# Optimization experiments

Hardware: AMD Instinct MI355X
Metric: run time of the kernel (lower is better)

Reference implementation:

```python
import jax, jax.numpy as jnp
import numpy as np
import math

D_MODEL = 768
NUM_HEADS = 12
HEAD_DIM = D_MODEL // NUM_HEADS
HIDDEN = 3072
EPS = 1e-05
CLAMP = 1e9


def setup_inputs() -> dict:
    key = jax.random.key(0)
    ks = jax.random.split(key, 8)
    s = 0.02
    return {
        "x": jax.random.normal(ks[0], (1, 4096, D_MODEL), dtype=jnp.float32),
        "gamma1": jnp.ones((D_MODEL,), jnp.float32),
        "beta1": jnp.zeros((D_MODEL,), jnp.float32),
        "Wqkv": jax.random.normal(ks[1], (D_MODEL, 3 * D_MODEL), jnp.float32) * s,
        "bqkv": jnp.zeros((3 * D_MODEL,), jnp.float32),
        "Wo": jax.random.normal(ks[2], (D_MODEL, D_MODEL), jnp.float32) * s,
        "bo": jnp.zeros((D_MODEL,), jnp.float32),
        "gamma2": jnp.ones((D_MODEL,), jnp.float32),
        "beta2": jnp.zeros((D_MODEL,), jnp.float32),
        "W1": jax.random.normal(ks[3], (D_MODEL, HIDDEN), jnp.float32) * s,
        "b1": jnp.zeros((HIDDEN,), jnp.float32),
        "W2": jax.random.normal(ks[4], (HIDDEN, D_MODEL), jnp.float32) * s,
        "b2": jnp.zeros((D_MODEL,), jnp.float32),
    }


def layer_norm(x, gamma, beta):
    mean = jnp.mean(x, axis=-1, keepdims=True)
    var = jnp.mean((x - mean) ** 2, axis=-1, keepdims=True)
    y = (x - mean) / jnp.sqrt(var + EPS)
    return gamma * y + beta


def attention_block(x, Wqkv, bqkv, Wo, bo):
    B, S, D = x.shape
    qkv = x @ Wqkv + bqkv                             # [B,S,3D]
    qkv = qkv.reshape(B, S, NUM_HEADS, 3 * HEAD_DIM).transpose(0, 2, 1, 3)  # [B,H,S,3hd]
    q, k, v = jnp.split(qkv, 3, axis=-1)              # each [B,H,S,hd]
    scaled = jnp.einsum("bhqd,bhkd->bhqk", q, k) / math.sqrt(HEAD_DIM)
    causal = jnp.tril(jnp.ones((S, S), dtype=bool))
    scaled = jnp.where(causal, scaled, -jnp.inf)
    scaled = jnp.clip(scaled, -CLAMP, CLAMP)          # torch clamp turns -inf into -1e9
    attn = jax.nn.softmax(scaled, axis=-1)
    vals = jnp.einsum("bhqk,bhkd->bhqd", attn, v)     # [B,H,S,hd]
    vals = vals.transpose(0, 2, 1, 3).reshape(B, S, D)
    return vals @ Wo + bo


def ffn_block(x, W1, b1, W2, b2):
    h = jax.nn.gelu(x @ W1 + b1, approximate=False)
    return h @ W2 + b2


def reference(x, gamma1, beta1, Wqkv, bqkv, Wo, bo, gamma2, beta2, W1, b1, W2, b2):
    x = x + attention_block(layer_norm(x, gamma1, beta1), Wqkv, bqkv, Wo, bo)
    x = x + ffn_block(layer_norm(x, gamma2, beta2), W1, b1, W2, b2)
    return x
```

## Files before the change

kernel.cpp:

```cpp
#include <hip/hip_runtime.h>
#include <hip/hip_bf16.h>
#include <cmath>

using u16 = unsigned short;
typedef __bf16 bf16x8 __attribute__((ext_vector_type(8)));
typedef __bf16 bf16x2 __attribute__((ext_vector_type(2)));
typedef unsigned short u16x8 __attribute__((ext_vector_type(8)));
typedef float f32x4 __attribute__((ext_vector_type(4)));

#define SEQ 4096
#define DM 768
#define NH 12
#define HD 64
#define HID 3072

__device__ __forceinline__ u16 f2bf(float f) {
    union { float f; unsigned u; } v; v.f = f;
    unsigned r = v.u + 0x7fffu + ((v.u >> 16) & 1u);
    return (u16)(r >> 16);
}

__device__ __forceinline__ unsigned pack_bf16(float a, float b) {
    union { bf16x2 v; unsigned u; } c;
    c.v[0] = (__bf16)a; c.v[1] = (__bf16)b;
    return c.u;
}

__device__ __forceinline__ float gelu_exact(float v) {
    float z = fabsf(v) * 0.70710678118654752f;
    float t = __builtin_amdgcn_rcpf(__builtin_fmaf(0.3275911f, z, 1.0f));
    float p = t * __builtin_fmaf(t, __builtin_fmaf(t, __builtin_fmaf(t,
                __builtin_fmaf(t, 1.061405429f, -1.453152027f),
                1.421413741f), -0.284496736f), 0.254829592f);
    float e = __builtin_amdgcn_exp2f(-z * z * 1.44269504088896341f);
    float erfv = __builtin_fmaf(-p, e, 1.0f);
    erfv = (v < 0.0f) ? -erfv : erfv;
    return 0.5f * v * (1.0f + erfv);
}

__device__ __forceinline__ int swz64(int row, int k) {
    return (row << 6) | ((((k >> 3) ^ row) & 7) << 3) | (k & 7);
}
__device__ __forceinline__ int swz128(int row, int k) {
    return (row << 7) | ((((k >> 3) ^ row) & 15) << 3) | (k & 7);
}

__device__ __forceinline__ void ln_row(const float* __restrict__ xr,
                                       const float* __restrict__ g,
                                       const float* __restrict__ b,
                                       u16* __restrict__ yr, int t) {
    float v0 = xr[t], v1 = xr[t + 256], v2 = xr[t + 512];
    float s = v0 + v1 + v2;
#pragma unroll
    for (int m = 32; m; m >>= 1) s += __shfl_xor(s, m);
    __shared__ float red[4], red2[4];
    int wid = t >> 6, lane = t & 63;
    if (lane == 0) red[wid] = s;
    __syncthreads();
    float mean = (red[0] + red[1] + red[2] + red[3]) * (1.0f / DM);
    float d0 = v0 - mean, d1 = v1 - mean, d2 = v2 - mean;
    float q = d0 * d0 + d1 * d1 + d2 * d2;
#pragma unroll
    for (int m = 32; m; m >>= 1) q += __shfl_xor(q, m);
    if (lane == 0) red2[wid] = q;
    __syncthreads();
    float var = (red2[0] + red2[1] + red2[2] + red2[3]) * (1.0f / DM);
    float rstd = rsqrtf(var + 1e-5f);
    yr[t]       = f2bf(d0 * rstd * g[t]       + b[t]);
    yr[t + 256] = f2bf(d1 * rstd * g[t + 256] + b[t + 256]);
    yr[t + 512] = f2bf(d2 * rstd * g[t + 512] + b[t + 512]);
}

__global__ __launch_bounds__(256) void prep_kernel(
    const float* __restrict__ x, const float* __restrict__ g1, const float* __restrict__ b1,
    const float* __restrict__ Wqkv, const float* __restrict__ Wo,
    const float* __restrict__ W1, const float* __restrict__ W2,
    u16* __restrict__ WqkvT, u16* __restrict__ WoT,
    u16* __restrict__ W1T, u16* __restrict__ W2T, u16* __restrict__ y) {
    int bid = blockIdx.x;
    if (bid < 6912) {
        const float* W; u16* Wt; int K, N, ntx, b;
        if (bid < 1728)      { W = Wqkv; Wt = WqkvT; K = 768;  N = 2304; ntx = 72; b = bid; }
        else if (bid < 2304) { W = Wo;   Wt = WoT;   K = 768;  N = 768;  ntx = 24; b = bid - 1728; }
        else if (bid < 4608) { W = W1;   Wt = W1T;   K = 768;  N = 3072; ntx = 96; b = bid - 2304; }
        else                 { W = W2;   Wt = W2T;   K = 3072; N = 768;  ntx = 24; b = bid - 4608; }
        int nb = (b % ntx) * 32, kb = (b / ntx) * 32;
        __shared__ float tile[32][33];
        int tx = threadIdx.x & 31, ty = threadIdx.x >> 5;
#pragma unroll
        for (int i = 0; i < 32; i += 8)
            tile[ty + i][tx] = W[(size_t)(kb + ty + i) * N + nb + tx];
        __syncthreads();
#pragma unroll
        for (int i = 0; i < 32; i += 8)
            Wt[(size_t)(nb + ty + i) * K + kb + tx] = f2bf(tile[tx][ty + i]);
    } else {
        int row = bid - 6912;
        ln_row(x + (size_t)row * DM, g1, b1, y + (size_t)row * DM, threadIdx.x);
    }
}

__global__ __launch_bounds__(256) void vtrans_kernel(const u16* __restrict__ qkv,
                                                     u16* __restrict__ VtG) {
    __shared__ u16 tile[64][68];
    int kvb = blockIdx.x;
    int h = blockIdx.y;
    int t = threadIdx.x;
    int r0 = t >> 3, c0 = (t & 7) << 3;
#pragma unroll
    for (int p = 0; p < 2; ++p) {
        u16x8 v = *reinterpret_cast<const u16x8*>(
            &qkv[(size_t)(kvb * 64 + r0 + p * 32) * 2304 + h * 192 + 128 + c0]);
#pragma unroll
        for (int j = 0; j < 8; ++j)
            tile[r0 + p * 32][c0 + j] = v[j];
    }
    __syncthreads();
    int kv = t & 63, db = (t >> 6) << 4;
#pragma unroll
    for (int i = 0; i < 16; ++i) {
        int d = db + i;
        VtG[(size_t)(h * 64 + d) * SEQ + kvb * 64 + kv] = tile[kv][d];
    }
}

__global__ __launch_bounds__(256) void ln_kernel(const float* __restrict__ x,
                                                 const float* __restrict__ g,
                                                 const float* __restrict__ b,
                                                 u16* __restrict__ y) {
    int row = blockIdx.x;
    ln_row(x + (size_t)row * DM, g, b, y + (size_t)row * DM, threadIdx.x);
}

template<int TM, int TN>
__global__ __launch_bounds__(256) void gemm_bf16(
    const u16* __restrict__ A, const u16* __restrict__ Bt,
    const float* __restrict__ bias, const float* __restrict__ resid,
    float* __restrict__ outF, u16* __restrict__ outB,
    int M, int N, int K, int gelu) {
    constexpr int AP = TM / 32;
    constexpr int BP = TN / 32;
    constexpr int MF = (TN == 128) ? 4 : 2;
    constexpr int NF = 2;
    __shared__ __align__(16) u16 As[2][TM * 64];
    __shared__ __align__(16) u16 Bs[2][TN * 64];
    int tid = threadIdx.x;
    int lane = tid & 63, wid = tid >> 6;
    int lr = lane & 15, hi = lane >> 4;
    int wrow = (TN == 128) ? 0 : (wid >> 1) * 32;
    int wcol = (TN == 128) ? wid * 32 : (wid & 1) * 32;
    int m0 = blockIdx.y * TM, n0 = blockIdx.x * TN;

    f32x4 acc[MF][NF] = {};
    int srow = tid >> 3;
    int sk = (tid & 7) << 3;
    const u16* Ag = A + (size_t)(m0 + srow) * K + sk;
    const u16* Bg = Bt + (size_t)(n0 + srow) * K + sk;

    u16x8 ar[AP], br[BP];
    auto LOAD = [&](int kt) {
#pragma unroll
        for (int p = 0; p < AP; ++p)
            ar[p] = *reinterpret_cast<const u16x8*>(Ag + (size_t)p * 32 * K + kt);
#pragma unroll
        for (int p = 0; p < BP; ++p)
            br[p] = *reinterpret_cast<const u16x8*>(Bg + (size_t)p * 32 * K + kt);
    };
    auto WRITE = [&](int buf) {
#pragma unroll
        for (int p = 0; p < AP; ++p)
            *reinterpret_cast<u16x8*>(&As[buf][swz64(srow + p * 32, sk)]) = ar[p];
#pragma unroll
        for (int p = 0; p < BP; ++p)
            *reinterpret_cast<u16x8*>(&Bs[buf][swz64(srow + p * 32, sk)]) = br[p];
    };

    int NT = K >> 6;
    LOAD(0);
    WRITE(0);
#pragma unroll 2
    for (int t = 0; t < NT; ++t) {
        if (t + 1 < NT) LOAD((t + 1) << 6);
        __syncthreads();
        const u16* as = &As[t & 1][0];
        const u16* bs = &Bs[t & 1][0];
#pragma unroll
        for (int ks = 0; ks < 2; ++ks) {
            bf16x8 af[MF], bfr[NF];
#pragma unroll
            for (int m = 0; m < MF; ++m)
                af[m] = *reinterpret_cast<const bf16x8*>(&as[swz64(wrow + m * 16 + lr, ks * 32 + hi * 8)]);
#pragma unroll
            for (int n = 0; n < NF; ++n)
                bfr[n] = *reinterpret_cast<const bf16x8*>(&bs[swz64(wcol + n * 16 + lr, ks * 32 + hi * 8)]);
            __builtin_amdgcn_s_setprio(1);
#pragma unroll
            for (int m = 0; m < MF; ++m)
#pragma unroll
                for (int n = 0; n < NF; ++n)
                    acc[m][n] = __builtin_amdgcn_mfma_f32_16x16x32_bf16(af[m], bfr[n], acc[m][n], 0, 0, 0);
            __builtin_amdgcn_s_setprio(0);
        }
        if (t + 1 < NT) WRITE((t + 1) & 1);
    }
#pragma unroll
    for (int m = 0; m < MF; ++m) {
#pragma unroll
        for (int n = 0; n < NF; ++n) {
            int col = n0 + wcol + n * 16 + lr;
            float bv = bias[col];
#pragma unroll
            for (int r = 0; r < 4; ++r) {
                int row = m0 + wrow + m * 16 + hi * 4 + r;
                float v = acc[m][n][r] + bv;
                if (gelu) v = gelu_exact(v);
                if (resid) v += resid[(size_t)row * N + col];
                if (outF) outF[(size_t)row * N + col] = v;
                if (outB) outB[(size_t)row * N + col] = f2bf(v);
            }
        }
    }
}

__global__ __launch_bounds__(256, 2) void attn_kernel(const u16* __restrict__ qkv,
                                                      const u16* __restrict__ VtG,
                                                      u16* __restrict__ attn) {
    __shared__ __align__(16) u16 Ks[2][128 * 64];
    __shared__ __align__(16) u16 Vt[2][64 * 128];
    int tid = threadIdx.x;
    int lane = tid & 63, w = tid >> 6;
    int lr = lane & 15, hi = lane >> 4;
    int upper = hi >> 1;
    const float SCL = 0.125f * 1.44269504088896340736f;

    int bid = blockIdx.x;
    int h = bid % NH;
    int qb = (SEQ / 64 - 1) - bid / NH;

    int qrow = qb * 64 + w * 16 + lr;
    bf16x8 qf[2];
#pragma unroll
    for (int ks = 0; ks < 2; ++ks)
        qf[ks] = *reinterpret_cast<const bf16x8*>(&qkv[(size_t)qrow * 2304 + h * 192 + ks * 32 + hi * 8]);

    f32x4 acc[4] = {};
    float m_run = -INFINITY, l_run = 0.0f;

    int skvr = tid >> 3;
    int skc = (tid & 7) << 3;
    int svd = tid >> 4;
    int svk = (tid & 15) << 3;
    u16x8 kr[4], vr[4];

    auto LOADKV = [&](int kb) {
#pragma unroll
        for (int p = 0; p < 4; ++p)
            kr[p] = *reinterpret_cast<const u16x8*>(
                &qkv[(size_t)(kb * 128 + skvr + p * 32) * 2304 + h * 192 + 64 + skc]);
#pragma unroll
        for (int p = 0; p < 4; ++p)
            vr[p] = *reinterpret_cast<const u16x8*>(
                &VtG[(size_t)(h * 64 + svd + p * 16) * SEQ + kb * 128 + svk]);
    };
    auto WRITEKV = [&](int buf) {
#pragma unroll
        for (int p = 0; p < 4; ++p)
            *reinterpret_cast<u16x8*>(&Ks[buf][swz64(skvr + p * 32, skc)]) = kr[p];
#pragma unroll
        for (int p = 0; p < 4; ++p)
            *reinterpret_cast<u16x8*>(&Vt[buf][swz128(svd + p * 16, svk)]) = vr[p];
    };

    int nt = (qb * 64 + 64 + 127) >> 7;
    LOADKV(0);
    WRITEKV(0);
    for (int kb = 0; kb < nt; ++kb) {
        if (kb + 1 < nt) LOADKV(kb + 1);
        __syncthreads();
        const u16* ksb = &Ks[kb & 1][0];
        const u16* vtb = &Vt[kb & 1][0];

        f32x4 s[8] = {};
        __builtin_amdgcn_s_setprio(1);
#pragma unroll
        for (int ks = 0; ks < 2; ++ks) {
#pragma unroll
            for (int n = 0; n < 8; ++n) {
                bf16x8 kf = *reinterpret_cast<const bf16x8*>(&ksb[swz64(n * 16 + lr, ks * 32 + hi * 8)]);
                s[n] = __builtin_amdgcn_mfma_f32_16x16x32_bf16(kf, qf[ks], s[n], 0, 0, 0);
            }
        }
        __builtin_amdgcn_s_setprio(0);
        float sv[8][4];
#pragma unroll
        for (int n = 0; n < 8; ++n) {
            sv[n][0] = s[n][0]; sv[n][1] = s[n][1]; sv[n][2] = s[n][2]; sv[n][3] = s[n][3];
        }
        if (kb == nt - 1) {
#pragma unroll
            for (int n = 0; n < 8; ++n)
#pragma unroll
                for (int r = 0; r < 4; ++r) {
                    int kv = kb * 128 + n * 16 + hi * 4 + r;
                    if (kv > qrow) sv[n][r] = -3.0e38f;
                }
        }
        float t8[8];
#pragma unroll
        for (int n = 0; n < 8; ++n)
            t8[n] = fmaxf(fmaxf(sv[n][0], sv[n][1]), fmaxf(sv[n][2], sv[n][3]));
        float mx = fmaxf(fmaxf(fmaxf(t8[0], t8[1]), fmaxf(t8[2], t8[3])),
                         fmaxf(fmaxf(t8[4], t8[5]), fmaxf(t8[6], t8[7])));
        mx = fmaxf(mx, __shfl_xor(mx, 16));
        mx = fmaxf(mx, __shfl_xor(mx, 32));
        float mxs = mx * SCL;
        if (!__all(mxs <= m_run + 8.0f)) {
            float mnew = fmaxf(m_run, mxs);
            float alpha = __builtin_amdgcn_exp2f(m_run - mnew);
            l_run *= alpha;
#pragma unroll
            for (int n2 = 0; n2 < 4; ++n2)
#pragma unroll
                for (int r = 0; r < 4; ++r) acc[n2][r] *= alpha;
            m_run = mnew;
        }
        float rs = 0.0f;
#pragma unroll
        for (int n = 0; n < 8; ++n) {
            float p0 = __builtin_amdgcn_exp2f(__builtin_fmaf(sv[n][0], SCL, -m_run));
            float p1 = __builtin_amdgcn_exp2f(__builtin_fmaf(sv[n][1], SCL, -m_run));
            float p2 = __builtin_amdgcn_exp2f(__builtin_fmaf(sv[n][2], SCL, -m_run));
            float p3 = __builtin_amdgcn_exp2f(__builtin_fmaf(sv[n][3], SCL, -m_run));
            sv[n][0] = p0; sv[n][1] = p1; sv[n][2] = p2; sv[n][3] = p3;
            rs += (p0 + p1) + (p2 + p3);
        }
        rs += __shfl_xor(rs, 16);
        rs += __shfl_xor(rs, 32);
        l_run += rs;

        unsigned pk0[8], pk1[8];
#pragma unroll
        for (int n = 0; n < 8; ++n) {
            pk0[n] = pack_bf16(sv[n][0], sv[n][1]);
            pk1[n] = pack_bf16(sv[n][2], sv[n][3]);
        }
        int src0 = lr + ((hi & 1) << 5);
        int src1 = src0 + 16;
#pragma unroll
        for (int ks = 0; ks < 4; ++ks) {
            union { unsigned w4[4]; bf16x8 v; } pf;
            {
                unsigned a0 = __shfl(pk0[2 * ks], src0), b0 = __shfl(pk0[2 * ks + 1], src0);
                unsigned a1 = __shfl(pk1[2 * ks], src0), b1 = __shfl(pk1[2 * ks + 1], src0);
                unsigned a2 = __shfl(pk0[2 * ks], src1), b2 = __shfl(pk0[2 * ks + 1], src1);
                unsigned a3 = __shfl(pk1[2 * ks], src1), b3 = __shfl(pk1[2 * ks + 1], src1);
                pf.w4[0] = upper ? b0 : a0;
                pf.w4[1] = upper ? b1 : a1;
                pf.w4[2] = upper ? b2 : a2;
                pf.w4[3] = upper ? b3 : a3;
            }
            __builtin_amdgcn_s_setprio(1);
#pragma unroll
            for (int n2 = 0; n2 < 4; ++n2) {
                bf16x8 vf = *reinterpret_cast<const bf16x8*>(&vtb[swz128(n2 * 16 + lr, ks * 32 + hi * 8)]);
                acc[n2] = __builtin_amdgcn_mfma_f32_16x16x32_bf16(vf, pf.v, acc[n2], 0, 0, 0);
            }
            __builtin_amdgcn_s_setprio(0);
        }
        if (kb + 1 < nt) WRITEKV((kb + 1) & 1);
    }
    float inv = 1.0f / l_run;
#pragma unroll
    for (int n2 = 0; n2 < 4; ++n2) {
#pragma unroll
        for (int r = 0; r < 4; ++r) {
            int dcol = h * 64 + n2 * 16 + hi * 4 + r;
            attn[(size_t)qrow * DM + dcol] = f2bf(acc[n2][r] * inv);
        }
    }
}

extern "C" void kernel_launch(void* const* d_in, const int* in_sizes, int n_in,
                              void* d_out, int out_size, void* d_ws, size_t ws_size,
                              hipStream_t stream) {
    const float* x      = (const float*)d_in[0];
    const float* gamma1 = (const float*)d_in[1];
    const float* beta1  = (const float*)d_in[2];
    const float* Wqkv   = (const float*)d_in[3];
    const float* bqkv   = (const float*)d_in[4];
    const float* Wo     = (const float*)d_in[5];
    const float* bo     = (const float*)d_in[6];
    const float* gamma2 = (const float*)d_in[7];
    const float* beta2  = (const float*)d_in[8];
    const float* W1     = (const float*)d_in[9];
    const float* b1     = (const float*)d_in[10];
    const float* W2     = (const float*)d_in[11];
    const float* b2     = (const float*)d_in[12];

    char* ws = (char*)d_ws;
    size_t off = 0;
    u16* WqkvT = (u16*)(ws + off); off += (size_t)2304 * 768 * 2;
    u16* WoT   = (u16*)(ws + off); off += (size_t)768 * 768 * 2;
    u16* W1T   = (u16*)(ws + off); off += (size_t)3072 * 768 * 2;
    u16* W2T   = (u16*)(ws + off); off += (size_t)768 * 3072 * 2;
    u16* B1    = (u16*)(ws + off); off += (size_t)SEQ * DM * 2;
    u16* Q     = (u16*)(ws + off); off += (size_t)SEQ * HID * 2;
    float* x1  = (float*)(ws + off); off += (size_t)SEQ * DM * 4;

    u16* VtG = (u16*)x1;

    prep_kernel<<<dim3(11008), 256, 0, stream>>>(x, gamma1, beta1, Wqkv, Wo, W1, W2,
                                                 WqkvT, WoT, W1T, W2T, B1);
    gemm_bf16<64, 128><<<dim3(2304 / 128, SEQ / 64), 256, 0, stream>>>(B1, WqkvT, bqkv, nullptr, nullptr, Q, SEQ, 2304, 768, 0);
    vtrans_kernel<<<dim3(SEQ / 64, NH), 256, 0, stream>>>(Q, VtG);
    attn_kernel<<<dim3((SEQ / 64) * NH), 256, 0, stream>>>(Q, VtG, B1);
    gemm_bf16<64, 64><<<dim3(768 / 64, SEQ / 64), 256, 0, stream>>>(B1, WoT, bo, x, x1, nullptr, SEQ, 768, 768, 0);
    ln_kernel<<<SEQ, 256, 0, stream>>>(x1, gamma2, beta2, B1);
    gemm_bf16<64, 128><<<dim3(3072 / 128, SEQ / 64), 256, 0, stream>>>(B1, W1T, b1, nullptr, nullptr, Q, SEQ, 3072, 768, 1);
    gemm_bf16<64, 64><<<dim3(768 / 64, SEQ / 64), 256, 0, stream>>>(Q, W2T, b2, x1, (float*)d_out, nullptr, SEQ, 768, 3072, 0);
}
```

Before: 207.4 us.

## Fuse V transpose into QKV GEMM epilogue and remap GEMM blocks for XCD locality

Removes the separate V-transpose kernel by having the QKV GEMM epilogue write the V columns transposed straight into the VtG buffer as 4-element vector stores. All GEMM launches switch to a 1D grid, with the block index remapped so that consecutive tiles are grouped across the 8 XCDs. This is meant to improve L2 reuse of shared A/B tiles. It saves one launch plus a read and write of V, in exchange for strided scattered stores in the GEMM epilogue.

```diff
diff --git a/kernel.cpp b/kernel.cpp
--- a/kernel.cpp
+++ b/kernel.cpp
@@ -6,6 +6,7 @@
 typedef __bf16 bf16x8 __attribute__((ext_vector_type(8)));
 typedef __bf16 bf16x2 __attribute__((ext_vector_type(2)));
 typedef unsigned short u16x8 __attribute__((ext_vector_type(8)));
+typedef unsigned short u16x4 __attribute__((ext_vector_type(4)));
 typedef float f32x4 __attribute__((ext_vector_type(4)));
 
 #define SEQ 4096
@@ -100,30 +101,6 @@
     }
 }
 
-__global__ __launch_bounds__(256) void vtrans_kernel(const u16* __restrict__ qkv,
-                                                     u16* __restrict__ VtG) {
-    __shared__ u16 tile[64][68];
-    int kvb = blockIdx.x;
-    int h = blockIdx.y;
-    int t = threadIdx.x;
-    int r0 = t >> 3, c0 = (t & 7) << 3;
-#pragma unroll
-    for (int p = 0; p < 2; ++p) {
-        u16x8 v = *reinterpret_cast<const u16x8*>(
-            &qkv[(size_t)(kvb * 64 + r0 + p * 32) * 2304 + h * 192 + 128 + c0]);
-#pragma unroll
-        for (int j = 0; j < 8; ++j)
-            tile[r0 + p * 32][c0 + j] = v[j];
-    }
-    __syncthreads();
-    int kv = t & 63, db = (t >> 6) << 4;
-#pragma unroll
-    for (int i = 0; i < 16; ++i) {
-        int d = db + i;
-        VtG[(size_t)(h * 64 + d) * SEQ + kvb * 64 + kv] = tile[kv][d];
-    }
-}
-
 __global__ __launch_bounds__(256) void ln_kernel(const float* __restrict__ x,
                                                  const float* __restrict__ g,
                                                  const float* __restrict__ b,
@@ -136,7 +113,7 @@
 __global__ __launch_bounds__(256) void gemm_bf16(
     const u16* __restrict__ A, const u16* __restrict__ Bt,
     const float* __restrict__ bias, const float* __restrict__ resid,
-    float* __restrict__ outF, u16* __restrict__ outB,
+    float* __restrict__ outF, u16* __restrict__ outB, u16* __restrict__ vtg,
     int M, int N, int K, int gelu) {
     constexpr int AP = TM / 32;
     constexpr int BP = TN / 32;
@@ -149,7 +126,11 @@
     int lr = lane & 15, hi = lane >> 4;
     int wrow = (TN == 128) ? 0 : (wid >> 1) * 32;
     int wcol = (TN == 128) ? wid * 32 : (wid & 1) * 32;
-    int m0 = blockIdx.y * TM, n0 = blockIdx.x * TN;
+
+    int nwg = gridDim.x;
+    int wg = (blockIdx.x & 7) * (nwg >> 3) + (blockIdx.x >> 3);
+    int nbx = N / TN;
+    int m0 = (wg / nbx) * TM, n0 = (wg % nbx) * TN;
 
     f32x4 acc[MF][NF] = {};
     int srow = tid >> 3;
@@ -209,14 +190,25 @@
         for (int n = 0; n < NF; ++n) {
             int col = n0 + wcol + n * 16 + lr;
             float bv = bias[col];
+            u16 q4[4];
 #pragma unroll
             for (int r = 0; r < 4; ++r) {
                 int row = m0 + wrow + m * 16 + hi * 4 + r;
                 float v = acc[m][n][r] + bv;
                 if (gelu) v = gelu_exact(v);
                 if (resid) v += resid[(size_t)row * N + col];
+                q4[r] = f2bf(v);
                 if (outF) outF[(size_t)row * N + col] = v;
-                if (outB) outB[(size_t)row * N + col] = f2bf(v);
+                if (outB) outB[(size_t)row * N + col] = q4[r];
+            }
+            if (vtg) {
+                int h = col / 192;
+                int c = col - h * 192;
+                if (c >= 128) {
+                    int row0 = m0 + wrow + m * 16 + hi * 4;
+                    u16x4 vv; vv[0] = q4[0]; vv[1] = q4[1]; vv[2] = q4[2]; vv[3] = q4[3];
+                    *reinterpret_cast<u16x4*>(&vtg[(size_t)(h * 64 + c - 128) * SEQ + row0]) = vv;
+                }
             }
         }
     }
@@ -411,11 +403,10 @@
 
     prep_kernel<<<dim3(11008), 256, 0, stream>>>(x, gamma1, beta1, Wqkv, Wo, W1, W2,
                                                  WqkvT, WoT, W1T, W2T, B1);
-    gemm_bf16<64, 128><<<dim3(2304 / 128, SEQ / 64), 256, 0, stream>>>(B1, WqkvT, bqkv, nullptr, nullptr, Q, SEQ, 2304, 768, 0);
-    vtrans_kernel<<<dim3(SEQ / 64, NH), 256, 0, stream>>>(Q, VtG);
+    gemm_bf16<64, 128><<<dim3(1152), 256, 0, stream>>>(B1, WqkvT, bqkv, nullptr, nullptr, Q, VtG, SEQ, 2304, 768, 0);
     attn_kernel<<<dim3((SEQ / 64) * NH), 256, 0, stream>>>(Q, VtG, B1);
-    gemm_bf16<64, 64><<<dim3(768 / 64, SEQ / 64), 256, 0, stream>>>(B1, WoT, bo, x, x1, nullptr, SEQ, 768, 768, 0);
+    gemm_bf16<64, 64><<<dim3(768), 256, 0, stream>>>(B1, WoT, bo, x, x1, nullptr, nullptr, SEQ, 768, 768, 0);
     ln_kernel<<<SEQ, 256, 0, stream>>>(x1, gamma2, beta2, B1);
-    gemm_bf16<64, 128><<<dim3(3072 / 128, SEQ / 64), 256, 0, stream>>>(B1, W1T, b1, nullptr, nullptr, Q, SEQ, 3072, 768, 1);
-    gemm_bf16<64, 64><<<dim3(768 / 64, SEQ / 64), 256, 0, stream>>>(Q, W2T, b2, x1, (float*)d_out, nullptr, SEQ, 768, 3072, 0);
-}
+    gemm_bf16<64, 128><<<dim3(1536), 256, 0, stream>>>(B1, W1T, b1, nullptr, nullptr, Q, nullptr, SEQ, 3072, 768, 1);
+    gemm_bf16<64, 64><<<dim3(768), 256, 0, stream>>>(Q, W2T, b2, x1, (float*)d_out, nullptr, nullptr, SEQ, 768, 3072, 0);
+}
```

Result: no change. 206.4 us, median of 2 (-0.5%).
